# Kernel optimization log

Measured on AMD Instinct MI355X. Metric: run time of the kernel, lower is better.

## Reference

```python
import jax, jax.numpy as jnp
import numpy as np

B, N, H = 4, 2048, 128
NUM_HEADS = 4
HEAD_DIM = H // NUM_HEADS
SCALE = np.sqrt(HEAD_DIM).astype(np.float32)


def setup_inputs() -> dict:
    key = jax.random.key(0)
    ks = jax.random.split(key, 16)

    def lin_w(k, o, i):
        return jax.random.normal(k, (o, i), dtype=jnp.float32) / np.sqrt(i).astype(np.float32)

    def lin_b(k, o, i):
        return jax.random.uniform(k, (o,), dtype=jnp.float32, minval=-1, maxval=1) / np.sqrt(i).astype(np.float32)

    return {
        "h": jax.random.normal(ks[0], (B, N, H), dtype=jnp.float32),
        "coords": jax.random.normal(ks[1], (B, N, 3), dtype=jnp.float32),
        "mask": jnp.ones((B, N), dtype=bool),
        "Wq": lin_w(ks[2], H, H), "bq": lin_b(ks[3], H, H),
        "Wk": lin_w(ks[4], H, H), "bk": lin_b(ks[5], H, H),
        "Wv": lin_w(ks[6], H, H), "bv": lin_b(ks[7], H, H),
        "Wo": lin_w(ks[8], H, H), "bo": lin_b(ks[9], H, H),
        "Wc1": lin_w(ks[10], H, H), "bc1": lin_b(ks[11], H, H),
        "Wc2": lin_w(ks[12], 1, H),  # no bias
    }


def reference(h, coords, mask, Wq, bq, Wk, bk, Wv, bv, Wo, bo, Wc1, bc1, Wc2):
    b, n, hd = h.shape
    # projections (torch Linear: y = x @ W.T + b), split heads
    Q = (h @ Wq.T + bq).reshape(b, n, NUM_HEADS, HEAD_DIM)
    K = (h @ Wk.T + bk).reshape(b, n, NUM_HEADS, HEAD_DIM)
    V = (h @ Wv.T + bv).reshape(b, n, NUM_HEADS, HEAD_DIM)

    # scores: (B, heads, N, N)
    scores = jnp.einsum('bnhd,bmhd->bhnm', Q, K) / SCALE
    # mask over keys (last dim), as in torch: mask (B,1,1,N)
    scores = jnp.where(mask[:, None, None, :], scores, -jnp.inf)
    attn = jax.nn.softmax(scores, axis=-1)  # dropout is identity in eval

    h_attn = jnp.einsum('bhnm,bmhd->bnhd', attn, V).reshape(b, n, hd)
    h_out = h_attn @ Wo.T + bo

    # scalar gate per node, softmax over nodes (dim=1)
    cw = jax.nn.silu(h @ Wc1.T + bc1) @ Wc2.T  # (B, N, 1)
    cw = jax.nn.softmax(cw, axis=1)

    # coords_update[b,n] = sum_m a[n,m]*(coords[n]-coords[m])
    #                    = (sum_m a[n,m]) * coords[n] - A @ coords
    # (avoids materializing the B x N x N x 3 coords_diff tensor; same math)
    attn_mean = attn.mean(axis=1)  # (B, N, N)
    row_sum = attn_mean.sum(axis=-1, keepdims=True)  # (B, N, 1)
    coords_update = row_sum * coords - jnp.einsum('bnm,bmd->bnd', attn_mean, coords)
    coords_out = coords + coords_update * cw
    return h_out, coords_out
```

## Files before the change

kernel.cpp:

```cpp
#include <hip/hip_runtime.h>
#include <hip/hip_bf16.h>


typedef __bf16    bf16x8 __attribute__((ext_vector_type(8)));
typedef __bf16    bf16x4 __attribute__((ext_vector_type(4)));
typedef _Float16  f16x8  __attribute__((ext_vector_type(8)));
typedef _Float16  f16x4  __attribute__((ext_vector_type(4)));
typedef float     f32x4  __attribute__((ext_vector_type(4)));

constexpr float QK_SCALE = 0.17677669529663687f;

__device__ inline bf16x8 cvt8(const float* p) {
    float4 a = *(const float4*)p;
    float4 b = *(const float4*)(p + 4);
    bf16x8 o;
    o[0] = (__bf16)a.x; o[1] = (__bf16)a.y; o[2] = (__bf16)a.z; o[3] = (__bf16)a.w;
    o[4] = (__bf16)b.x; o[5] = (__bf16)b.y; o[6] = (__bf16)b.z; o[7] = (__bf16)b.w;
    return o;
}

__global__ __launch_bounds__(256) void prep(
    const float* __restrict__ h, const float* __restrict__ coords,
    const float* __restrict__ Wq, const float* __restrict__ Wk,
    const float* __restrict__ Wv, const float* __restrict__ Wc1,
    const float* __restrict__ Wo,
    __hip_bfloat16* __restrict__ hsw2, __hip_bfloat16* __restrict__ Wsw,
    _Float16* __restrict__ Csw)
{
    const int tid = threadIdx.x, blk = blockIdx.x;
    if (blk < 512) {
        int k4 = tid >> 6, lane = tid & 63;
        int col = lane & 15, quad = lane >> 4;
        bf16x8 o = cvt8(h + (size_t)(blk * 16 + col) * 128 + k4 * 32 + quad * 8);
        *(bf16x8*)(hsw2 + ((size_t)(blk * 4 + k4) * 64 + lane) * 8) = o;
    } else if (blk < 552) {
        int lin = (blk - 512) * 256 + tid;
        int lane = lin & 63, rest = lin >> 6;
        int sub = rest & 7, mk = rest >> 3;
        int mat = mk >> 2, k4 = mk & 3;
        int col = lane & 15, quad = lane >> 4;
        const float* W = (mat == 0) ? Wq : (mat == 1) ? Wk :
                         (mat == 2) ? Wv : (mat == 3) ? Wc1 : Wo;
        bf16x8 o = cvt8(W + (size_t)(sub * 16 + col) * 128 + k4 * 32 + quad * 8);
        *(bf16x8*)(Wsw + (size_t)lin * 8) = o;
    } else {
        int lin = (blk - 552) * 256 + tid;
        int lane = lin & 63, bk2 = lin >> 6;
        int col = lane & 15, quad = lane >> 4;
        f16x4 o;
        if (col < 3) {
            #pragma unroll
            for (int j = 0; j < 4; ++j)
                o[j] = (_Float16)coords[((size_t)bk2 * 16 + quad * 4 + j) * 3 + col];
        } else if (col == 3) {
            o[0] = o[1] = o[2] = o[3] = (_Float16)1.f;
        } else {
            o[0] = o[1] = o[2] = o[3] = (_Float16)0.f;
        }
        *(f16x4*)(Csw + (size_t)lin * 4) = o;
    }
}

__global__ __launch_bounds__(256) void proj_mfma(
    const __hip_bfloat16* __restrict__ hsw2, const __hip_bfloat16* __restrict__ Wsw,
    const float* __restrict__ bq, const float* __restrict__ bk,
    const float* __restrict__ bv, const float* __restrict__ bc1,
    const float* __restrict__ Wc2,
    __hip_bfloat16* __restrict__ Qb, __hip_bfloat16* __restrict__ Kb,
    _Float16* __restrict__ Vsw, float* __restrict__ g)
{
    const int tid = threadIdx.x;
    const int wave = tid >> 6, lane = tid & 63;
    const int col = lane & 15, quad = lane >> 4;
    const int row0 = blockIdx.x * 16;
    const int b = row0 >> 11, n0 = row0 & 2047;

    bf16x8 a[4];
    #pragma unroll
    for (int k4 = 0; k4 < 4; ++k4)
        a[k4] = *(const bf16x8*)(hsw2 + ((size_t)(blockIdx.x * 4 + k4) * 64 + lane) * 8);

    f32x4 acc[8];
    #pragma unroll
    for (int s = 0; s < 8; ++s) acc[s] = (f32x4){0.f, 0.f, 0.f, 0.f};

    #pragma unroll
    for (int k4 = 0; k4 < 4; ++k4) {
        #pragma unroll
        for (int sub = 0; sub < 8; ++sub) {
            bf16x8 bf = *(const bf16x8*)(Wsw +
                (((size_t)(wave * 4 + k4) * 8 + sub) * 64 + lane) * 8);
            acc[sub] = __builtin_amdgcn_mfma_f32_16x16x32_bf16(a[k4], bf, acc[sub], 0, 0, 0);
        }
    }

    if (wave == 0) {
        #pragma unroll
        for (int sub = 0; sub < 8; ++sub) {
            int c = sub * 16 + col, head = c >> 5, d = c & 31;
            float bias = bq[c];
            size_t base = (size_t)(b * 4 + head) * 2048 + n0 + quad * 4;
            #pragma unroll
            for (int r = 0; r < 4; ++r)
                Qb[(base + r) * 32 + d] = __float2bfloat16((acc[sub][r] + bias) * QK_SCALE);
        }
    } else if (wave == 1) {
        #pragma unroll
        for (int sub = 0; sub < 8; ++sub) {
            int c = sub * 16 + col, head = c >> 5, d = c & 31;
            float bias = bk[c];
            size_t base = (size_t)(b * 4 + head) * 2048 + n0 + quad * 4;
            #pragma unroll
            for (int r = 0; r < 4; ++r)
                Kb[(base + r) * 32 + d] = __float2bfloat16(acc[sub][r] + bias);
        }
    } else if (wave == 2) {
        const int kc = n0 >> 4;
        #pragma unroll
        for (int sub = 0; sub < 8; ++sub) {
            int c = sub * 16 + col, head = c >> 5;
            float bias = bv[c];
            f16x4 vv;
            #pragma unroll
            for (int r = 0; r < 4; ++r) vv[r] = (_Float16)(acc[sub][r] + bias);
            *(f16x4*)(Vsw + (((size_t)(b * 4 + head) * 128 + kc) * 64
                             + quad * 16 + col) * 8 + (sub & 1) * 4) = vv;
        }
    } else {
        float gsum[4] = {0.f, 0.f, 0.f, 0.f};
        #pragma unroll
        for (int sub = 0; sub < 8; ++sub) {
            int c = sub * 16 + col;
            float bias = bc1[c], w2 = Wc2[c];
            #pragma unroll
            for (int r = 0; r < 4; ++r) {
                float x = acc[sub][r] + bias;
                gsum[r] += (x / (1.f + __expf(-x))) * w2;
            }
        }
        #pragma unroll
        for (int r = 0; r < 4; ++r) {
            gsum[r] += __shfl_xor(gsum[r], 1);
            gsum[r] += __shfl_xor(gsum[r], 2);
            gsum[r] += __shfl_xor(gsum[r], 4);
            gsum[r] += __shfl_xor(gsum[r], 8);
            if (col == 0) g[row0 + quad * 4 + r] = gsum[r];
        }
    }
}

__global__ __launch_bounds__(256, 4) void attn_mfma(
    const __hip_bfloat16* __restrict__ Qb, const __hip_bfloat16* __restrict__ Kb,
    const _Float16* __restrict__ Vsw, const _Float16* __restrict__ Csw,
    __hip_bfloat16* __restrict__ hsw, float* __restrict__ Ach)
{
    __shared__ f32x4 red[6][4][64];

    const int tid = threadIdx.x;
    const int wave = tid >> 6, lane = tid & 63;
    const int col = lane & 15, quad = lane >> 4;
    const int bh = blockIdx.y, b = bh >> 2, head = bh & 3;
    const int q0 = blockIdx.x * 32;

    const __hip_bfloat16* Qp = Qb + ((size_t)bh * 2048 + q0) * 32;
    const bf16x8 qA = *(const bf16x8*)(Qp + (size_t)col * 32 + quad * 8);
    const bf16x8 qB = *(const bf16x8*)(Qp + (size_t)(16 + col) * 32 + quad * 8);

    const __hip_bfloat16* Kp = Kb + ((size_t)bh * 2048 + wave * 512) * 32;
    const _Float16* Vp = Vsw + ((size_t)bh * 128 + wave * 32) * 512;
    const _Float16* Cp = Csw + ((size_t)b * 128 + wave * 32) * 256;

    f32x4 oLoA = {0,0,0,0}, oHiA = {0,0,0,0}, cA = {0,0,0,0};
    f32x4 oLoB = {0,0,0,0}, oHiB = {0,0,0,0}, cB = {0,0,0,0};
    const f32x4 fz = {0,0,0,0};

    #pragma unroll 4
    for (int it = 0; it < 32; ++it) {
        bf16x8 kf = *(const bf16x8*)(Kp + (size_t)(it * 16 + col) * 32 + quad * 8);
        f16x8 v8  = *(const f16x8*)(Vp + (size_t)it * 512 + lane * 8);
        f16x4 cf  = *(const f16x4*)(Cp + (size_t)it * 256 + lane * 4);

        f32x4 sA = __builtin_amdgcn_mfma_f32_16x16x32_bf16(kf, qA, fz, 0, 0, 0);
        f32x4 sB = __builtin_amdgcn_mfma_f32_16x16x32_bf16(kf, qB, fz, 0, 0, 0);

        f16x4 pA, pB;
        #pragma unroll
        for (int r = 0; r < 4; ++r) {
            pA[r] = (_Float16)__expf(sA[r]);
            pB[r] = (_Float16)__expf(sB[r]);
        }

        f16x4 vlo = {v8[0], v8[1], v8[2], v8[3]};
        f16x4 vhi = {v8[4], v8[5], v8[6], v8[7]};

        oLoA = __builtin_amdgcn_mfma_f32_16x16x16f16(vlo, pA, oLoA, 0, 0, 0);
        oHiA = __builtin_amdgcn_mfma_f32_16x16x16f16(vhi, pA, oHiA, 0, 0, 0);
        cA   = __builtin_amdgcn_mfma_f32_16x16x16f16(cf,  pA, cA,   0, 0, 0);
        oLoB = __builtin_amdgcn_mfma_f32_16x16x16f16(vlo, pB, oLoB, 0, 0, 0);
        oHiB = __builtin_amdgcn_mfma_f32_16x16x16f16(vhi, pB, oHiB, 0, 0, 0);
        cB   = __builtin_amdgcn_mfma_f32_16x16x16f16(cf,  pB, cB,   0, 0, 0);
    }

    red[0][wave][lane] = oLoA; red[1][wave][lane] = oHiA; red[2][wave][lane] = cA;
    red[3][wave][lane] = oLoB; red[4][wave][lane] = oHiB; red[5][wave][lane] = cB;
    __syncthreads();
    if (wave >= 2) return;

    const int base = wave * 3;
    f32x4 oLo = red[base+0][0][lane], oHi = red[base+1][0][lane], cc = red[base+2][0][lane];
    #pragma unroll
    for (int w = 1; w < 4; ++w) {
        oLo += red[base+0][w][lane];
        oHi += red[base+1][w][lane];
        cc  += red[base+2][w][lane];
    }
    float l = red[base+2][0][col][3] + red[base+2][1][col][3] +
              red[base+2][2][col][3] + red[base+2][3][col][3];
    float invl = 1.f / l;

    const int t = (b * 2048 + q0) / 16 + wave;
    bf16x4 lo4, hi4;
    #pragma unroll
    for (int r = 0; r < 4; ++r) {
        lo4[r] = (__bf16)(oLo[r] * invl);
        hi4[r] = (__bf16)(oHi[r] * invl);
    }
    *(bf16x4*)(hsw + ((size_t)(t * 4 + head) * 64 + (quad >> 1) * 16 + col) * 8
                    + (quad & 1) * 4) = lo4;
    *(bf16x4*)(hsw + ((size_t)(t * 4 + head) * 64 + (2 + (quad >> 1)) * 16 + col) * 8
                    + (quad & 1) * 4) = hi4;

    if (quad == 0) {
        const int q = q0 + wave * 16 + col;
        #pragma unroll
        for (int r = 0; r < 3; ++r)
            Ach[((size_t)bh * 2048 + q) * 3 + r] = cc[r] * invl;
    }
}

__global__ __launch_bounds__(256) void gate_softmax(
    const float* __restrict__ g, float* __restrict__ cw)
{
    __shared__ float red[256];
    const int b = blockIdx.x, tid = threadIdx.x;
    const float* gb = g + b * 2048;
    float mx = -1e30f;
    for (int n = tid; n < 2048; n += 256) mx = fmaxf(mx, gb[n]);
    red[tid] = mx; __syncthreads();
    for (int s = 128; s > 0; s >>= 1) {
        if (tid < s) red[tid] = fmaxf(red[tid], red[tid + s]);
        __syncthreads();
    }
    float M = red[0];
    __syncthreads();
    float sum = 0.f;
    for (int n = tid; n < 2048; n += 256) sum += __expf(gb[n] - M);
    red[tid] = sum; __syncthreads();
    for (int s = 128; s > 0; s >>= 1) {
        if (tid < s) red[tid] += red[tid + s];
        __syncthreads();
    }
    float invS = 1.f / red[0];
    for (int n = tid; n < 2048; n += 256)
        cw[b * 2048 + n] = __expf(gb[n] - M) * invS;
}

__global__ __launch_bounds__(256) void out_mfma(
    const __hip_bfloat16* __restrict__ hsw, const __hip_bfloat16* __restrict__ Wsw,
    const float* __restrict__ bo, const float* __restrict__ coords,
    const float* __restrict__ Ach, const float* __restrict__ cw,
    float* __restrict__ out_h, float* __restrict__ out_c)
{
    const int tid = threadIdx.x;
    const int wave = tid >> 6, lane = tid & 63;
    const int col = lane & 15, quad = lane >> 4;
    const int t = blockIdx.x, row0 = t * 16;

    bf16x8 a[4];
    #pragma unroll
    for (int k4 = 0; k4 < 4; ++k4)
        a[k4] = *(const bf16x8*)(hsw + ((size_t)(t * 4 + k4) * 64 + lane) * 8);

    f32x4 acc[2] = {{0.f,0.f,0.f,0.f}, {0.f,0.f,0.f,0.f}};
    #pragma unroll
    for (int k4 = 0; k4 < 4; ++k4) {
        #pragma unroll
        for (int sub = 0; sub < 2; ++sub) {
            int c16 = wave * 2 + sub;
            bf16x8 bf = *(const bf16x8*)(Wsw +
                (((size_t)(16 + k4) * 8 + c16) * 64 + lane) * 8);
            acc[sub] = __builtin_amdgcn_mfma_f32_16x16x32_bf16(a[k4], bf, acc[sub], 0, 0, 0);
        }
    }

    #pragma unroll
    for (int sub = 0; sub < 2; ++sub) {
        int c = (wave * 2 + sub) * 16 + col;
        float bias = bo[c];
        #pragma unroll
        for (int r = 0; r < 4; ++r)
            out_h[(size_t)(row0 + quad * 4 + r) * 128 + c] = acc[sub][r] + bias;
    }

    if (tid < 48) {
        int r = tid / 3, d2 = tid % 3;
        size_t row = (size_t)row0 + r;
        int b = (int)(row >> 11), nloc = (int)(row & 2047);
        float am = 0.f;
        #pragma unroll
        for (int hh = 0; hh < 4; ++hh)
            am += Ach[((size_t)(b * 4 + hh) * 2048 + nloc) * 3 + d2];
        am *= 0.25f;
        float c = coords[row * 3 + d2];
        out_c[row * 3 + d2] = c + (c - am) * cw[row];
    }
}

extern "C" void kernel_launch(void* const* d_in, const int* in_sizes, int n_in,
                              void* d_out, int out_size, void* d_ws, size_t ws_size,
                              hipStream_t stream)
{
    (void)in_sizes; (void)n_in; (void)out_size; (void)ws_size;

    const float* h      = (const float*)d_in[0];
    const float* coords = (const float*)d_in[1];
    const float* Wq  = (const float*)d_in[3];  const float* bq  = (const float*)d_in[4];
    const float* Wk  = (const float*)d_in[5];  const float* bk  = (const float*)d_in[6];
    const float* Wv  = (const float*)d_in[7];  const float* bv  = (const float*)d_in[8];
    const float* Wo  = (const float*)d_in[9];  const float* bo  = (const float*)d_in[10];
    const float* Wc1 = (const float*)d_in[11]; const float* bc1 = (const float*)d_in[12];
    const float* Wc2 = (const float*)d_in[13];

    __hip_bfloat16* hsw2 = (__hip_bfloat16*)d_ws;
    __hip_bfloat16* Qb   = hsw2 + 1048576;
    __hip_bfloat16* Kb   = Qb + 1048576;
    __hip_bfloat16* hsw  = Kb + 1048576;
    __hip_bfloat16* Wsw  = hsw + 1048576;
    _Float16* Vsw = (_Float16*)(Wsw + 81920);
    _Float16* Csw = Vsw + 1048576;
    float* fp  = (float*)(Csw + 131072);
    float* g   = fp;
    float* cw  = fp + 8192;
    float* Ach = fp + 16384;

    float* out_h = (float*)d_out;
    float* out_c = out_h + (size_t)4 * 2048 * 128;

    hipLaunchKernelGGL(prep, dim3(680), dim3(256), 0, stream,
                       h, coords, Wq, Wk, Wv, Wc1, Wo, hsw2, Wsw, Csw);
    hipLaunchKernelGGL(proj_mfma, dim3(512), dim3(256), 0, stream,
                       hsw2, Wsw, bq, bk, bv, bc1, Wc2, Qb, Kb, Vsw, g);
    hipLaunchKernelGGL(attn_mfma, dim3(64, 16), dim3(256), 0, stream,
                       Qb, Kb, Vsw, Csw, hsw, Ach);
    hipLaunchKernelGGL(gate_softmax, dim3(4), dim3(256), 0, stream, g, cw);
    hipLaunchKernelGGL(out_mfma, dim3(512), dim3(256), 0, stream,
                       hsw, Wsw, bo, coords, Ach, cw, out_h, out_c);
}
```

Measured before the change: 118.1 us.

## Prefetch K/V/C tiles in attention loop and fuse gate softmax into output kernel

The attention loop now software-pipelines its global loads of K, V and coordinate fragments three iterations ahead using a four-slot register ring buffer, so memory latency can overlap the MFMA and exp work. Separately, the standalone gate softmax kernel is removed: each out_mfma block recomputes the per-batch max and sum of the 2048 gate logits with wave shuffles and shared memory, then forms the gate weight inline. This drops one kernel launch and the cw round trip through memory, at the cost of redundant reductions in every block and higher register pressure in the attention kernel.

```diff
diff --git a/kernel.cpp b/kernel.cpp
--- a/kernel.cpp
+++ b/kernel.cpp
@@ -174,11 +174,26 @@
     f32x4 oLoB = {0,0,0,0}, oHiB = {0,0,0,0}, cB = {0,0,0,0};
     const f32x4 fz = {0,0,0,0};
 
+    bf16x8 kbuf[4]; f16x8 vbuf[4]; f16x4 cbuf[4];
+    #pragma unroll
+    for (int s = 0; s < 3; ++s) {
+        kbuf[s] = *(const bf16x8*)(Kp + (size_t)(s * 16 + col) * 32 + quad * 8);
+        vbuf[s] = *(const f16x8*)(Vp + (size_t)s * 512 + lane * 8);
+        cbuf[s] = *(const f16x4*)(Cp + (size_t)s * 256 + lane * 4);
+    }
+
     #pragma unroll 4
     for (int it = 0; it < 32; ++it) {
-        bf16x8 kf = *(const bf16x8*)(Kp + (size_t)(it * 16 + col) * 32 + quad * 8);
-        f16x8 v8  = *(const f16x8*)(Vp + (size_t)it * 512 + lane * 8);
-        f16x4 cf  = *(const f16x4*)(Cp + (size_t)it * 256 + lane * 4);
+        const int pf = (it + 3 < 32) ? (it + 3) : 31;
+        const int ws2 = (it + 3) & 3;
+        kbuf[ws2] = *(const bf16x8*)(Kp + (size_t)(pf * 16 + col) * 32 + quad * 8);
+        vbuf[ws2] = *(const f16x8*)(Vp + (size_t)pf * 512 + lane * 8);
+        cbuf[ws2] = *(const f16x4*)(Cp + (size_t)pf * 256 + lane * 4);
+
+        const int rs = it & 3;
+        bf16x8 kf = kbuf[rs];
+        f16x8 v8  = vbuf[rs];
+        f16x4 cf  = cbuf[rs];
 
         f32x4 sA = __builtin_amdgcn_mfma_f32_16x16x32_bf16(kf, qA, fz, 0, 0, 0);
         f32x4 sB = __builtin_amdgcn_mfma_f32_16x16x32_bf16(kf, qB, fz, 0, 0, 0);
@@ -238,43 +253,37 @@
     }
 }
 
-__global__ __launch_bounds__(256) void gate_softmax(
-    const float* __restrict__ g, float* __restrict__ cw)
-{
-    __shared__ float red[256];
-    const int b = blockIdx.x, tid = threadIdx.x;
-    const float* gb = g + b * 2048;
-    float mx = -1e30f;
-    for (int n = tid; n < 2048; n += 256) mx = fmaxf(mx, gb[n]);
-    red[tid] = mx; __syncthreads();
-    for (int s = 128; s > 0; s >>= 1) {
-        if (tid < s) red[tid] = fmaxf(red[tid], red[tid + s]);
-        __syncthreads();
-    }
-    float M = red[0];
-    __syncthreads();
-    float sum = 0.f;
-    for (int n = tid; n < 2048; n += 256) sum += __expf(gb[n] - M);
-    red[tid] = sum; __syncthreads();
-    for (int s = 128; s > 0; s >>= 1) {
-        if (tid < s) red[tid] += red[tid + s];
-        __syncthreads();
-    }
-    float invS = 1.f / red[0];
-    for (int n = tid; n < 2048; n += 256)
-        cw[b * 2048 + n] = __expf(gb[n] - M) * invS;
-}
-
 __global__ __launch_bounds__(256) void out_mfma(
     const __hip_bfloat16* __restrict__ hsw, const __hip_bfloat16* __restrict__ Wsw,
     const float* __restrict__ bo, const float* __restrict__ coords,
-    const float* __restrict__ Ach, const float* __restrict__ cw,
+    const float* __restrict__ Ach, const float* __restrict__ g,
     float* __restrict__ out_h, float* __restrict__ out_c)
 {
+    __shared__ float sred[8];
+
     const int tid = threadIdx.x;
     const int wave = tid >> 6, lane = tid & 63;
     const int col = lane & 15, quad = lane >> 4;
     const int t = blockIdx.x, row0 = t * 16;
+    const int b = row0 >> 11;
+    const float* gb = g + (size_t)b * 2048;
+
+    float4 g0 = *(const float4*)(gb + tid * 8);
+    float4 g1 = *(const float4*)(gb + tid * 8 + 4);
+    float mx = fmaxf(fmaxf(fmaxf(g0.x, g0.y), fmaxf(g0.z, g0.w)),
+                     fmaxf(fmaxf(g1.x, g1.y), fmaxf(g1.z, g1.w)));
+    #pragma unroll
+    for (int off = 32; off; off >>= 1) mx = fmaxf(mx, __shfl_xor(mx, off));
+    if (lane == 0) sred[wave] = mx;
+    __syncthreads();
+    float M = fmaxf(fmaxf(sred[0], sred[1]), fmaxf(sred[2], sred[3]));
+    float sum = __expf(g0.x - M) + __expf(g0.y - M) + __expf(g0.z - M) + __expf(g0.w - M)
+              + __expf(g1.x - M) + __expf(g1.y - M) + __expf(g1.z - M) + __expf(g1.w - M);
+    #pragma unroll
+    for (int off = 32; off; off >>= 1) sum += __shfl_xor(sum, off);
+    if (lane == 0) sred[4 + wave] = sum;
+    __syncthreads();
+    float invS = 1.f / (sred[4] + sred[5] + sred[6] + sred[7]);
 
     bf16x8 a[4];
     #pragma unroll
@@ -305,14 +314,15 @@
     if (tid < 48) {
         int r = tid / 3, d2 = tid % 3;
         size_t row = (size_t)row0 + r;
-        int b = (int)(row >> 11), nloc = (int)(row & 2047);
+        int nloc = (int)(row & 2047);
         float am = 0.f;
         #pragma unroll
         for (int hh = 0; hh < 4; ++hh)
             am += Ach[((size_t)(b * 4 + hh) * 2048 + nloc) * 3 + d2];
         am *= 0.25f;
+        float cwv = __expf(gb[nloc] - M) * invS;
         float c = coords[row * 3 + d2];
-        out_c[row * 3 + d2] = c + (c - am) * cw[row];
+        out_c[row * 3 + d2] = c + (c - am) * cwv;
     }
 }
 
@@ -340,8 +350,7 @@
     _Float16* Csw = Vsw + 1048576;
     float* fp  = (float*)(Csw + 131072);
     float* g   = fp;
-    float* cw  = fp + 8192;
-    float* Ach = fp + 16384;
+    float* Ach = fp + 8192;
 
     float* out_h = (float*)d_out;
     float* out_c = out_h + (size_t)4 * 2048 * 128;
@@ -352,7 +361,6 @@
                        hsw2, Wsw, bq, bk, bv, bc1, Wc2, Qb, Kb, Vsw, g);
     hipLaunchKernelGGL(attn_mfma, dim3(64, 16), dim3(256), 0, stream,
                        Qb, Kb, Vsw, Csw, hsw, Ach);
-    hipLaunchKernelGGL(gate_softmax, dim3(4), dim3(256), 0, stream, g, cw);
     hipLaunchKernelGGL(out_mfma, dim3(512), dim3(256), 0, stream,
-                       hsw, Wsw, bo, coords, Ach, cw, out_h, out_c);
-}
+                       hsw, Wsw, bo, coords, Ach, g, out_h, out_c);
+}
```

After: 113.7 us. 3.7% less time.
